# Kernel tuning notes

Hardware: AMD Instinct MI355X
Metric: run time of the kernel (lower is better)

## Reference

```python
import jax, jax.numpy as jnp
import numpy as np

EPS = 1e-5

def splice(x, offsets):
    # x: [B, F, T]; offsets already shifted so offsets[0] == 0.
    # Output channel order matches torch reshape(-1, C*F): y[b, f*C+c, t] = x[b, f, t+off[c]]
    w = offsets[-1]
    Tn = x.shape[2] - w
    y = jnp.stack([x[:, :, o:o + Tn] for o in offsets], axis=2)  # [B, F, C, Tn]
    B, F, C, _ = y.shape
    return y.reshape(B, F * C, Tn)

def conv1x1(x, w, b):
    # x: [B, Cin, T], w: [Cout, Cin], b: [Cout]
    return jnp.einsum('oc,bct->bot', w, x) + b[None, :, None]

def bn_ct(x, gamma=None, beta=None):
    # BatchNorm1d (training mode, biased var) over (batch, time) per channel
    m = x.mean(axis=(0, 2), keepdims=True)
    v = x.var(axis=(0, 2), keepdims=True)
    y = (x - m) * jax.lax.rsqrt(v + EPS)
    if gamma is not None:
        y = y * gamma[None, :, None] + beta[None, :, None]
    return y

def bn_c(x, gamma, beta):
    # BatchNorm1d on [B, C]
    m = x.mean(axis=0, keepdims=True)
    v = x.var(axis=0, keepdims=True)
    return (x - m) * jax.lax.rsqrt(v + EPS) * gamma[None, :] + beta[None, :]

def relu6(x):
    return jnp.clip(x, 0.0, 6.0)

def setup_inputs() -> dict:
    key = jax.random.key(0)
    ks = list(jax.random.split(key, 32))
    def rn(shape, scale=0.05):
        return jax.random.normal(ks.pop(), shape, dtype=jnp.float32) * scale
    inp = {
        'x': jax.random.normal(ks.pop(), (32, 2048, 20), dtype=jnp.float32),
        'h1_w': rn((512, 100)), 'h1_b': rn((512,)),
        'h2_w': rn((512, 1536)), 'h2_b': rn((512,)),
        'bn2_g': jnp.ones((512,), jnp.float32), 'bn2_b': jnp.zeros((512,), jnp.float32),
        'h3_w': rn((512, 1536)), 'h3_b': rn((512,)),
        'bn3_g': jnp.ones((512,), jnp.float32), 'bn3_b': jnp.zeros((512,), jnp.float32),
        'h4_w': rn((512, 512)), 'h4_b': rn((512,)),
        'bn4_g': jnp.ones((512,), jnp.float32), 'bn4_b': jnp.zeros((512,), jnp.float32),
        'h5_w': rn((1500, 512)), 'h5_b': rn((1500,)),
        'bn5_g': jnp.ones((1500,), jnp.float32), 'bn5_b': jnp.zeros((1500,), jnp.float32),
        'l1_w': rn((512, 3000)), 'l1_b': rn((512,)),
        'bn6_g': jnp.ones((512,), jnp.float32), 'bn6_b': jnp.zeros((512,), jnp.float32),
        'l2_w': rn((512, 512)), 'l2_b': rn((512,)),
        'bn7_g': jnp.ones((512,), jnp.float32), 'bn7_b': jnp.zeros((512,), jnp.float32),
    }
    return inp

def reference(x, h1_w, h1_b, h2_w, h2_b, bn2_g, bn2_b, h3_w, h3_b, bn3_g, bn3_b,
              h4_w, h4_b, bn4_g, bn4_b, h5_w, h5_b, bn5_g, bn5_b,
              l1_w, l1_b, bn6_g, bn6_b, l2_w, l2_b, bn7_g, bn7_b):
    o = jnp.transpose(x, (0, 2, 1))                     # [B, 20, T]
    o = splice(o, (0, 1, 2, 3, 4))                      # context [-2..2] -> [B, 100, T-4]
    o = bn_ct(jax.nn.relu(conv1x1(o, h1_w, h1_b)))      # bn1 affine=False
    o = splice(o, (0, 2, 4))                            # context [-2,0,2] -> [B, 1536, T-8]
    o = bn_ct(jax.nn.relu(conv1x1(o, h2_w, h2_b)), bn2_g, bn2_b)
    o = splice(o, (0, 3, 6))                            # context [-3,0,3] -> [B, 1536, T-14]
    o = bn_ct(jax.nn.relu(conv1x1(o, h3_w, h3_b)), bn3_g, bn3_b)
    o = bn_ct(relu6(conv1x1(o, h4_w, h4_b)), bn4_g, bn4_b)
    o = bn_ct(relu6(conv1x1(o, h5_w, h5_b)), bn5_g, bn5_b)  # [B, 1500, T']
    mean = o.mean(axis=-1)
    std = jnp.std(o, axis=-1, ddof=1)                   # torch.std is unbiased
    o = jnp.concatenate((mean, std), axis=1)            # [B, 3000]
    o = bn_c(relu6(o @ l1_w.T + l1_b), bn6_g, bn6_b)
    o = bn_c(relu6(o @ l2_w.T + l2_b), bn7_g, bn7_b)
    return o
```

## Files before the change

### kernel.cpp

```cpp
#include <hip/hip_runtime.h>
#include <cstdint>

#define EPSF 1e-5f

namespace {

typedef _Float16 f16;
typedef _Float16 v8h __attribute__((ext_vector_type(8)));
typedef float v4f __attribute__((ext_vector_type(4)));

constexpr int B  = 32;
constexpr int T0 = 2048, F0 = 20;
constexpr int T1 = 2044, T2 = 2040, T3 = 2034;
constexpr int TS = 2048;

__device__ __forceinline__ void gload16(const void* g, void* l) {
    typedef const __attribute__((address_space(1))) void* gp_t;
    typedef __attribute__((address_space(3))) void* lp_t;
    __builtin_amdgcn_global_load_lds((gp_t)(unsigned long long)g,
                                     (lp_t)(unsigned int)(unsigned long long)l,
                                     16, 0, 0);
}
__device__ __forceinline__ void wait_vm4() { asm volatile("s_waitcnt vmcnt(4)" ::: "memory"); }
__device__ __forceinline__ void wait_vm0() { asm volatile("s_waitcnt vmcnt(0)" ::: "memory"); }

__global__ __launch_bounds__(256) void transpose_x(const float* __restrict__ x,
                                                   f16* __restrict__ xT,
                                                   float* __restrict__ stZ)
{
    int idx = blockIdx.x * 256 + threadIdx.x;
    if (idx < 4096) stZ[idx] = 0.f;
    constexpr int total = B * 3 * TS * 8;
    if (idx >= total) return;
    int fl = idx & 7;
    int t  = (idx >> 3) & (TS - 1);
    int fo = (idx >> 14) % 3;
    int b  = idx / (3 << 14);
    int f  = fo * 8 + fl;
    float v = (f < F0) ? x[((size_t)b * T0 + t) * F0 + f] : 0.f;
    xT[idx] = (f16)v;
}

template<int FP, int C>
__global__ __launch_bounds__(256) void fold_mfma(
    const float* __restrict__ W, const float* __restrict__ bias,
    const float* __restrict__ st, const float* __restrict__ gamma, const float* __restrict__ beta,
    f16* __restrict__ Wh, float* __restrict__ bf,
    int Oreal, int Freal, int Cin, int CinOrig, float invN)
{
    int o = blockIdx.x;
    auto sidx = [&](int k) {
        return ((size_t)((o >> 7) * (Cin >> 3) + (k >> 3)) * 128 + (o & 127)) * 8 + (k & 7);
    };
    if (o >= Oreal) {
        for (int k = threadIdx.x; k < Cin; k += 256) Wh[sidx(k)] = (f16)0.f;
        if (threadIdx.x == 0) bf[o] = 0.f;
        return;
    }
    float local = 0.f;
    for (int k = threadIdx.x; k < Cin; k += 256) {
        int c = k / FP, f = k - c * FP;
        float wv = 0.f;
        if (c < C && f < Freal) {
            float sc = 1.f, sh = 0.f;
            if (st) {
                float mean = st[f] * invN;
                float var  = st[Freal + f] * invN - mean * mean;
                sc = rsqrtf(var + EPSF);
                if (gamma) sc *= gamma[f];
                sh = (beta ? beta[f] : 0.f) - mean * sc;
            }
            float w = W[(size_t)o * CinOrig + f * C + c];
            wv = w * sc;
            local += w * sh;
        }
        Wh[sidx(k)] = (f16)wv;
    }
#pragma unroll
    for (int d = 32; d; d >>= 1) local += __shfl_down(local, d);
    __shared__ float red[4];
    if ((threadIdx.x & 63) == 0) red[threadIdx.x >> 6] = local;
    __syncthreads();
    if (threadIdx.x == 0) bf[o] = bias[o] + red[0] + red[1] + red[2] + red[3];
}

template<int ACT, int FPR, int CIN>
__global__ __launch_bounds__(256, 4) void conv_mfma(
    const f16* __restrict__ inT, const f16* __restrict__ Wh,
    const float* __restrict__ bias, f16* __restrict__ outT,
    float* __restrict__ st, int O, int Tout, int offMul)
{
    __shared__ __align__(16) f16 Ilds[2][4 * 128 * 8];
    __shared__ __align__(16) f16 Wlds[2][4 * 128 * 8];
    __shared__ float redS[2][128];
    __shared__ float redQ[2][128];
    const int tid  = threadIdx.x;
    const int lane = tid & 63, wave = tid >> 6;
    const int wt = wave & 1, wo = wave >> 1;
    const int quad = lane >> 4, l16 = lane & 15;
    const int tB = blockIdx.x * 128, oB = blockIdx.y * 128, b = blockIdx.z;
    const f16* inb = inT + (size_t)b * FPR * TS;
    const size_t wBase = (size_t)(oB >> 7) * (CIN >> 3);

    v4f acc[4][4];
#pragma unroll
    for (int mi = 0; mi < 4; ++mi)
#pragma unroll
        for (int ni = 0; ni < 4; ++ni)
#pragma unroll
            for (int r = 0; r < 4; ++r) acc[mi][ni][r] = 0.f;

    constexpr int nIter = CIN >> 5;

    auto compute = [&](int pb) {
        v8h afr[4], bfr[4];
#pragma unroll
        for (int mi = 0; mi < 4; ++mi)
            afr[mi] = *(const v8h*)&Ilds[pb][(quad * 128 + wt * 64 + mi * 16 + l16) * 8];
#pragma unroll
        for (int ni = 0; ni < 4; ++ni)
            bfr[ni] = *(const v8h*)&Wlds[pb][(quad * 128 + wo * 64 + ni * 16 + l16) * 8];
#pragma unroll
        for (int mi = 0; mi < 4; ++mi)
#pragma unroll
            for (int ni = 0; ni < 4; ++ni)
                acc[mi][ni] = __builtin_amdgcn_mfma_f32_16x16x32_f16(
                    afr[mi], bfr[ni], acc[mi][ni], 0, 0, 0);
    };

    if constexpr (FPR == 512) {
        const char* gp0;
        const char* gp1;
        intptr_t dN, dWr;
        if (wave < 2) {
            gp0 = (const char*)(inb + ((size_t)(2 * wave) * TS + tB + lane) * 8);
            gp1 = gp0 + (size_t)TS * 16;
            dN  = (intptr_t)4 * TS * 16;
            dWr = ((intptr_t)(-60) * TS + offMul) * 16;
        } else {
            gp0 = (const char*)(Wh + ((wBase + 2 * (wave - 2)) * 128 + lane) * 8);
            gp1 = gp0;
            dN  = 8192;
            dWr = 8192;
        }
        auto stage_fast = [&](int pb) {
            f16* Ib = &Ilds[pb][0];
            f16* Wb = &Wlds[pb][0];
            if (wave < 2) {
                int k0 = 2 * wave;
                gload16(gp0,        Ib + (k0 * 128) * 8);
                gload16(gp0 + 1024, Ib + (k0 * 128 + 64) * 8);
                gload16(gp1,        Ib + ((k0 + 1) * 128) * 8);
                gload16(gp1 + 1024, Ib + ((k0 + 1) * 128 + 64) * 8);
            } else {
                int k0 = 2 * (wave - 2);
                gload16(gp0,        Wb + (k0 * 128) * 8);
                gload16(gp0 + 1024, Wb + (k0 * 128 + 64) * 8);
                gload16(gp0 + 2048, Wb + ((k0 + 1) * 128) * 8);
                gload16(gp0 + 3072, Wb + ((k0 + 1) * 128 + 64) * 8);
            }
        };
        auto advance = [&](int kFrom) {
            intptr_t d = (((kFrom + 1) & 15) == 0) ? dWr : dN;
            gp0 += d;
            if (wave < 2) gp1 += d;
        };

        stage_fast(0);
        advance(0);
#pragma unroll 2
        for (int k = 0; k < nIter; ++k) {
            const int pb = k & 1;
            __syncthreads();
            if (k + 1 < nIter) { stage_fast(pb ^ 1); advance(k + 1); wait_vm4(); }
            else               { wait_vm0(); }
            __syncthreads();
            compute(pb);
        }
    } else {
        auto stage = [&](int iB, int pb) {
#pragma unroll
            for (int j = 0; j < 4; ++j) {
                int s = wave * 4 + j;
                int koct = (s & 7) >> 1, half = s & 1;
                if (s < 8) {
                    int kidx = iB + koct * 8;
                    int c = kidx / FPR, f = kidx - c * FPR;
                    int t = tB + half * 64 + lane + c * offMul;
                    gload16(inb + ((size_t)(f >> 3) * TS + t) * 8,
                            &Ilds[pb][(koct * 128 + half * 64) * 8]);
                } else {
                    gload16(Wh + ((wBase + (iB >> 3) + koct) * 128 + half * 64 + lane) * 8,
                            &Wlds[pb][(koct * 128 + half * 64) * 8]);
                }
            }
        };
        stage(0, 0);
#pragma unroll 2
        for (int k = 0; k < nIter; ++k) {
            const int pb = k & 1;
            __syncthreads();
            if (k + 1 < nIter) { stage((k + 1) * 32, pb ^ 1); wait_vm4(); }
            else               { wait_vm0(); }
            __syncthreads();
            compute(pb);
        }
    }

    float Sl[4] = {0, 0, 0, 0}, Ql[4] = {0, 0, 0, 0};
#pragma unroll
    for (int ni = 0; ni < 4; ++ni) {
        const int o  = oB + wo * 64 + ni * 16 + l16;
        const float bs = bias[o];
        f16* orow = outT + (size_t)b * O * TS + (size_t)(o >> 3) * TS * 8 + (o & 7);
#pragma unroll
        for (int mi = 0; mi < 4; ++mi)
#pragma unroll
            for (int r = 0; r < 4; ++r) {
                int t = tB + wt * 64 + mi * 16 + quad * 4 + r;
                if (t < Tout) {
                    float v = acc[mi][ni][r] + bs;
                    v = fmaxf(v, 0.f);
                    if (ACT == 2) v = fminf(v, 6.f);
                    orow[(size_t)t * 8] = (f16)v;
                    Sl[ni] += v; Ql[ni] += v * v;
                }
            }
    }
#pragma unroll
    for (int ni = 0; ni < 4; ++ni) {
        float s = Sl[ni], q = Ql[ni];
        s += __shfl_down(s, 32); q += __shfl_down(q, 32);
        s += __shfl_down(s, 16); q += __shfl_down(q, 16);
        if (lane < 16) {
            redS[wt][wo * 64 + ni * 16 + lane] = s;
            redQ[wt][wo * 64 + ni * 16 + lane] = q;
        }
    }
    __syncthreads();
    if (tid < 128) {
        atomicAdd(&st[oB + tid],       redS[0][tid] + redS[1][tid]);
        atomicAdd(&st[512 + oB + tid], redQ[0][tid] + redQ[1][tid]);
    }
}

template<int CIN>
__global__ __launch_bounds__(256, 4) void pool_mfma(
    const f16* __restrict__ inT, const f16* __restrict__ Wh,
    const float* __restrict__ bias, float* __restrict__ Sp, float* __restrict__ Qp,
    int T, int Opad)
{
    const int L    = blockIdx.x;
    const int slot = L >> 3;
    const int oB   = (slot % 12) * 128;
    const int cz   = (L & 7) + 8 * (slot / 12);
    const int b    = cz & 31, z = cz >> 5;

    __shared__ __align__(16) f16 Ilds[2][4 * 128 * 8];
    __shared__ __align__(16) f16 Wlds[2][4 * 128 * 8];
    __shared__ float redS[2][128];
    __shared__ float redQ[2][128];
    const int tid  = threadIdx.x;
    const int lane = tid & 63, wave = tid >> 6;
    const int wt = wave & 1, wo = wave >> 1;
    const int quad = lane >> 4, l16 = lane & 15;
    const f16* inb = inT + (size_t)b * CIN * TS;
    const size_t wBase = (size_t)(oB >> 7) * (CIN >> 3);

    float Sl[4] = {0, 0, 0, 0}, Ql[4] = {0, 0, 0, 0};
    float bs[4];
#pragma unroll
    for (int ni = 0; ni < 4; ++ni) bs[ni] = bias[oB + wo * 64 + ni * 16 + l16];

    const int tBase = z * 256;
    constexpr int kPer  = CIN >> 5;
    constexpr int total = 2 * kPer;

    v4f acc[4][4];
#pragma unroll
    for (int mi = 0; mi < 4; ++mi)
#pragma unroll
        for (int ni = 0; ni < 4; ++ni)
#pragma unroll
            for (int r = 0; r < 4; ++r) acc[mi][ni][r] = 0.f;

    const char* gp0;
    const char* gp1;
    intptr_t dN, dWr;
    if (wave < 2) {
        gp0 = (const char*)(inb + ((size_t)(2 * wave) * TS + tBase + lane) * 8);
        gp1 = gp0 + (size_t)TS * 16;
        dN  = (intptr_t)4 * TS * 16;
        dWr = ((intptr_t)(-60) * TS + 128) * 16;
    } else {
        gp0 = (const char*)(Wh + ((wBase + 2 * (wave - 2)) * 128 + lane) * 8);
        gp1 = gp0;
        dN  = 8192;
        dWr = (intptr_t)(-60) * 128 * 16;
    }
    auto stage_fast = [&](int pb) {
        f16* Ib = &Ilds[pb][0];
        f16* Wb = &Wlds[pb][0];
        if (wave < 2) {
            int k0 = 2 * wave;
            gload16(gp0,        Ib + (k0 * 128) * 8);
            gload16(gp0 + 1024, Ib + (k0 * 128 + 64) * 8);
            gload16(gp1,        Ib + ((k0 + 1) * 128) * 8);
            gload16(gp1 + 1024, Ib + ((k0 + 1) * 128 + 64) * 8);
        } else {
            int k0 = 2 * (wave - 2);
            gload16(gp0,        Wb + (k0 * 128) * 8);
            gload16(gp0 + 1024, Wb + (k0 * 128 + 64) * 8);
            gload16(gp0 + 2048, Wb + ((k0 + 1) * 128) * 8);
            gload16(gp0 + 3072, Wb + ((k0 + 1) * 128 + 64) * 8);
        }
    };
    auto advance = [&](int itFrom) {
        intptr_t d = (((itFrom + 1) & 15) == 0) ? dWr : dN;
        gp0 += d;
        if (wave < 2) gp1 += d;
    };

    stage_fast(0);
    advance(0);
#pragma unroll 2
    for (int it = 0; it < total; ++it) {
        const int pb = it & 1;
        __syncthreads();
        if (it + 1 < total) { stage_fast(pb ^ 1); advance(it + 1); wait_vm4(); }
        else                { wait_vm0(); }
        __syncthreads();
        v8h afr[4], bfr[4];
#pragma unroll
        for (int mi = 0; mi < 4; ++mi)
            afr[mi] = *(const v8h*)&Ilds[pb][(quad * 128 + wt * 64 + mi * 16 + l16) * 8];
#pragma unroll
        for (int ni = 0; ni < 4; ++ni)
            bfr[ni] = *(const v8h*)&Wlds[pb][(quad * 128 + wo * 64 + ni * 16 + l16) * 8];
#pragma unroll
        for (int mi = 0; mi < 4; ++mi)
#pragma unroll
            for (int ni = 0; ni < 4; ++ni)
                acc[mi][ni] = __builtin_amdgcn_mfma_f32_16x16x32_f16(
                    afr[mi], bfr[ni], acc[mi][ni], 0, 0, 0);

        if ((it & (kPer - 1)) == kPer - 1) {
            int tB = tBase + (it >> 4) * 128;
#pragma unroll
            for (int ni = 0; ni < 4; ++ni)
#pragma unroll
                for (int mi = 0; mi < 4; ++mi)
#pragma unroll
                    for (int r = 0; r < 4; ++r) {
                        int t = tB + wt * 64 + mi * 16 + quad * 4 + r;
                        if (t < T) {
                            float v = fminf(fmaxf(acc[mi][ni][r] + bs[ni], 0.f), 6.f);
                            Sl[ni] += v; Ql[ni] += v * v;
                        }
                        acc[mi][ni][r] = 0.f;
                    }
        }
    }

#pragma unroll
    for (int ni = 0; ni < 4; ++ni) {
        float s = Sl[ni], q = Ql[ni];
        s += __shfl_down(s, 32); q += __shfl_down(q, 32);
        s += __shfl_down(s, 16); q += __shfl_down(q, 16);
        if (lane < 16) {
            redS[wt][wo * 64 + ni * 16 + lane] = s;
            redQ[wt][wo * 64 + ni * 16 + lane] = q;
        }
    }
    __syncthreads();
    if (tid < 128) {
        int o = oB + tid;
        Sp[((size_t)z * B + b) * Opad + o] = redS[0][tid] + redS[1][tid];
        Qp[((size_t)z * B + b) * Opad + o] = redQ[0][tid] + redQ[1][tid];
    }
}

__global__ __launch_bounds__(256) void pool_finalize(
    const float* __restrict__ Sp, const float* __restrict__ Qp,
    const float* __restrict__ g5, const float* __restrict__ b5,
    float* __restrict__ stat, int Opad, int Oreal, int T)
{
    int wid  = (blockIdx.x * 256 + threadIdx.x) >> 6;
    int lane = threadIdx.x & 63;
    if (wid >= Oreal) return;
    const int co = wid;
    const int b  = lane & 31, zh = lane >> 5;
    double sb = 0, qb = 0;
#pragma unroll
    for (int zz = 0; zz < 4; ++zz) {
        int z = zh + 2 * zz;
        sb += Sp[((size_t)z * B + b) * Opad + co];
        qb += Qp[((size_t)z * B + b) * Opad + co];
    }
    sb += __shfl_xor(sb, 32);
    qb += __shfl_xor(qb, 32);
    double sS = sb, sQ = qb;
#pragma unroll
    for (int d = 16; d; d >>= 1) { sS += __shfl_xor(sS, d); sQ += __shfl_xor(sQ, d); }
    double invN = 1.0 / ((double)B * T);
    double m = sS * invN;
    double v = sQ * invN - m * m;
    float sc = g5[co] * rsqrtf((float)v + EPSF);
    float sh = b5[co] - (float)m * sc;
    if (lane < 32) {
        double mb = sb / T;
        double vb = (qb - sb * sb / T) / (T - 1);
        if (vb < 0) vb = 0;
        stat[(size_t)b * 2 * Oreal + co]         = (float)mb * sc + sh;
        stat[(size_t)b * 2 * Oreal + Oreal + co] = sqrtf((float)vb) * fabsf(sc);
    }
}

__global__ __launch_bounds__(256) void fc_relu6(const float* __restrict__ x,
                                                const float* __restrict__ W,
                                                const float* __restrict__ bias,
                                                float* __restrict__ y, int Cin, int O)
{
    int wid = (blockIdx.x * 256 + threadIdx.x) >> 6;
    int lane = threadIdx.x & 63;
    if (wid >= B * O) return;
    int b = wid / O, o = wid - b * O;
    const float* xr = x + (size_t)b * Cin;
    const float* wr = W + (size_t)o * Cin;
    float s = 0.f;
    for (int c = lane; c < Cin; c += 64) s = fmaf(xr[c], wr[c], s);
#pragma unroll
    for (int d = 32; d; d >>= 1) s += __shfl_down(s, d);
    if (lane == 0) y[wid] = fminf(fmaxf(s + bias[o], 0.f), 6.f);
}

__global__ __launch_bounds__(512) void bn_batch(const float* __restrict__ x,
                                                const float* __restrict__ g,
                                                const float* __restrict__ be,
                                                float* __restrict__ y, int O)
{
    int o = threadIdx.x;
    if (o >= O) return;
    float s = 0.f, q = 0.f;
    for (int b = 0; b < B; ++b) { float v = x[b * O + o]; s += v; q += v * v; }
    float m = s / B;
    float var = q / B - m * m;
    float sc = g[o] * rsqrtf(var + EPSF);
    float sh = be[o] - m * sc;
    for (int b = 0; b < B; ++b) y[b * O + o] = x[b * O + o] * sc + sh;
}

}

extern "C" void kernel_launch(void* const* d_in, const int* in_sizes, int n_in,
                              void* d_out, int out_size, void* d_ws, size_t ws_size,
                              hipStream_t stream)
{
    (void)in_sizes; (void)n_in; (void)out_size; (void)ws_size;
    const float* x     = (const float*)d_in[0];
    const float* h1_w  = (const float*)d_in[1];
    const float* h1_b  = (const float*)d_in[2];
    const float* h2_w  = (const float*)d_in[3];
    const float* h2_b  = (const float*)d_in[4];
    const float* bn2_g = (const float*)d_in[5];
    const float* bn2_b = (const float*)d_in[6];
    const float* h3_w  = (const float*)d_in[7];
    const float* h3_b  = (const float*)d_in[8];
    const float* bn3_g = (const float*)d_in[9];
    const float* bn3_b = (const float*)d_in[10];
    const float* h4_w  = (const float*)d_in[11];
    const float* h4_b  = (const float*)d_in[12];
    const float* bn4_g = (const float*)d_in[13];
    const float* bn4_b = (const float*)d_in[14];
    const float* h5_w  = (const float*)d_in[15];
    const float* h5_b  = (const float*)d_in[16];
    const float* bn5_g = (const float*)d_in[17];
    const float* bn5_b = (const float*)d_in[18];
    const float* l1_w  = (const float*)d_in[19];
    const float* l1_b  = (const float*)d_in[20];
    const float* bn6_g = (const float*)d_in[21];
    const float* bn6_b = (const float*)d_in[22];
    const float* l2_w  = (const float*)d_in[23];
    const float* l2_b  = (const float*)d_in[24];
    const float* bn7_g = (const float*)d_in[25];
    const float* bn7_b = (const float*)d_in[26];

    char* ws = (char*)d_ws;
    size_t off = 0;
    auto alloc = [&](size_t bytes) {
        char* p = ws + off;
        off += (bytes + 255) & ~(size_t)255;
        return (void*)p;
    };
    f16* xT    = (f16*)alloc(((size_t)B * 3  * TS * 8 + 2048) * 2);
    f16* bufA  = (f16*)alloc(((size_t)B * 64 * TS * 8 + 2048) * 2);
    f16* bufB  = (f16*)alloc(((size_t)B * 64 * TS * 8 + 2048) * 2);
    f16* Wh1   = (f16*)alloc((size_t)512 * 128 * 2);
    f16* Wh2   = (f16*)alloc((size_t)512 * 1536 * 2);
    f16* Wh3   = (f16*)alloc((size_t)512 * 1536 * 2);
    f16* Wh4   = (f16*)alloc((size_t)512 * 512 * 2);
    f16* Wh5   = (f16*)alloc((size_t)1536 * 512 * 2);
    float* bf1 = (float*)alloc(512 * 4);
    float* bf2 = (float*)alloc(512 * 4);
    float* bf3 = (float*)alloc(512 * 4);
    float* bf4 = (float*)alloc(512 * 4);
    float* bf5 = (float*)alloc(1536 * 4);
    float* stZ = (float*)alloc(4096 * 4);
    float* st1 = stZ, *st2 = stZ + 1024, *st3 = stZ + 2048, *st4 = stZ + 3072;
    float* Sp  = (float*)alloc((size_t)8 * B * 1536 * 4);
    float* Qp  = (float*)alloc((size_t)8 * B * 1536 * 4);
    float* stat = (float*)alloc((size_t)B * 3000 * 4);
    float* f1  = (float*)alloc((size_t)B * 512 * 4);
    float* f2  = (float*)alloc((size_t)B * 512 * 4);

    transpose_x<<<(B * 3 * TS * 8 + 255) / 256, 256, 0, stream>>>(x, xT, stZ);

    fold_mfma<24, 5><<<512, 256, 0, stream>>>(h1_w, h1_b, nullptr, nullptr, nullptr,
                                              Wh1, bf1, 512, 20, 128, 100, 0.f);
    conv_mfma<1, 24, 128><<<dim3(16, 4, B), 256, 0, stream>>>(
        xT, Wh1, bf1, bufA, st1, 512, T1, 1);

    fold_mfma<512, 3><<<512, 256, 0, stream>>>(h2_w, h2_b, st1, nullptr, nullptr,
                                               Wh2, bf2, 512, 512, 1536, 1536,
                                               1.f / (B * T1));
    conv_mfma<1, 512, 1536><<<dim3(16, 4, B), 256, 0, stream>>>(
        bufA, Wh2, bf2, bufB, st2, 512, T2, 2);

    fold_mfma<512, 3><<<512, 256, 0, stream>>>(h3_w, h3_b, st2, bn2_g, bn2_b,
                                               Wh3, bf3, 512, 512, 1536, 1536,
                                               1.f / (B * T2));
    conv_mfma<1, 512, 1536><<<dim3(16, 4, B), 256, 0, stream>>>(
        bufB, Wh3, bf3, bufA, st3, 512, T3, 3);

    fold_mfma<512, 1><<<512, 256, 0, stream>>>(h4_w, h4_b, st3, bn3_g, bn3_b,
                                               Wh4, bf4, 512, 512, 512, 512,
                                               1.f / (B * T3));
    conv_mfma<2, 512, 512><<<dim3(16, 4, B), 256, 0, stream>>>(
        bufA, Wh4, bf4, bufB, st4, 512, T3, 0);

    fold_mfma<512, 1><<<1536, 256, 0, stream>>>(h5_w, h5_b, st4, bn4_g, bn4_b,
                                                Wh5, bf5, 1500, 512, 512, 512,
                                                1.f / (B * T3));
    pool_mfma<512><<<3072, 256, 0, stream>>>(bufB, Wh5, bf5, Sp, Qp, T3, 1536);

    pool_finalize<<<(1500 * 64 + 255) / 256, 256, 0, stream>>>(
        Sp, Qp, bn5_g, bn5_b, stat, 1536, 1500, T3);

    fc_relu6<<<(B * 512 * 64 + 255) / 256, 256, 0, stream>>>(stat, l1_w, l1_b, f1, 3000, 512);
    bn_batch<<<1, 512, 0, stream>>>(f1, bn6_g, bn6_b, f1, 512);
    fc_relu6<<<(B * 512 * 64 + 255) / 256, 256, 0, stream>>>(f1, l2_w, l2_b, f2, 512, 512);
    bn_batch<<<1, 512, 0, stream>>>(f2, bn7_g, bn7_b, (float*)d_out, 512);
}
```

Baseline: 641.6 us.

## Load MFMA operands directly from global memory into registers, bypassing LDS staging

Adds conv_reg and pool_reg kernels where each wave loads its A and W fragments straight from global memory into registers. This replaces the double-buffered global_load_lds staging with its two barriers per iteration. The 512-channel layers and the pooling layer now use these kernels. The conv_mfma fast path is removed, and conv_mfma stays only for layer 1. This removes the LDS traffic and barrier stalls, but each wave now loads its own copy of data the block previously shared, so global and L2 traffic rise and latency hiding depends on unrolling.

```diff
diff --git a/kernel.cpp b/kernel.cpp
--- a/kernel.cpp
+++ b/kernel.cpp
@@ -128,83 +128,32 @@
                     afr[mi], bfr[ni], acc[mi][ni], 0, 0, 0);
     };
 
-    if constexpr (FPR == 512) {
-        const char* gp0;
-        const char* gp1;
-        intptr_t dN, dWr;
-        if (wave < 2) {
-            gp0 = (const char*)(inb + ((size_t)(2 * wave) * TS + tB + lane) * 8);
-            gp1 = gp0 + (size_t)TS * 16;
-            dN  = (intptr_t)4 * TS * 16;
-            dWr = ((intptr_t)(-60) * TS + offMul) * 16;
-        } else {
-            gp0 = (const char*)(Wh + ((wBase + 2 * (wave - 2)) * 128 + lane) * 8);
-            gp1 = gp0;
-            dN  = 8192;
-            dWr = 8192;
+    auto stage = [&](int iB, int pb) {
+#pragma unroll
+        for (int j = 0; j < 4; ++j) {
+            int s = wave * 4 + j;
+            int koct = (s & 7) >> 1, half = s & 1;
+            if (s < 8) {
+                int kidx = iB + koct * 8;
+                int c = kidx / FPR, f = kidx - c * FPR;
+                int t = tB + half * 64 + lane + c * offMul;
+                gload16(inb + ((size_t)(f >> 3) * TS + t) * 8,
+                        &Ilds[pb][(koct * 128 + half * 64) * 8]);
+            } else {
+                gload16(Wh + ((wBase + (iB >> 3) + koct) * 128 + half * 64 + lane) * 8,
+                        &Wlds[pb][(koct * 128 + half * 64) * 8]);
+            }
         }
-        auto stage_fast = [&](int pb) {
-            f16* Ib = &Ilds[pb][0];
-            f16* Wb = &Wlds[pb][0];
-            if (wave < 2) {
-                int k0 = 2 * wave;
-                gload16(gp0,        Ib + (k0 * 128) * 8);
-                gload16(gp0 + 1024, Ib + (k0 * 128 + 64) * 8);
-                gload16(gp1,        Ib + ((k0 + 1) * 128) * 8);
-                gload16(gp1 + 1024, Ib + ((k0 + 1) * 128 + 64) * 8);
-            } else {
-                int k0 = 2 * (wave - 2);
-                gload16(gp0,        Wb + (k0 * 128) * 8);
-                gload16(gp0 + 1024, Wb + (k0 * 128 + 64) * 8);
-                gload16(gp0 + 2048, Wb + ((k0 + 1) * 128) * 8);
-                gload16(gp0 + 3072, Wb + ((k0 + 1) * 128 + 64) * 8);
-            }
-        };
-        auto advance = [&](int kFrom) {
-            intptr_t d = (((kFrom + 1) & 15) == 0) ? dWr : dN;
-            gp0 += d;
-            if (wave < 2) gp1 += d;
-        };
-
-        stage_fast(0);
-        advance(0);
+    };
+    stage(0, 0);
 #pragma unroll 2
-        for (int k = 0; k < nIter; ++k) {
-            const int pb = k & 1;
-            __syncthreads();
-            if (k + 1 < nIter) { stage_fast(pb ^ 1); advance(k + 1); wait_vm4(); }
-            else               { wait_vm0(); }
-            __syncthreads();
-            compute(pb);
-        }
-    } else {
-        auto stage = [&](int iB, int pb) {
-#pragma unroll
-            for (int j = 0; j < 4; ++j) {
-                int s = wave * 4 + j;
-                int koct = (s & 7) >> 1, half = s & 1;
-                if (s < 8) {
-                    int kidx = iB + koct * 8;
-                    int c = kidx / FPR, f = kidx - c * FPR;
-                    int t = tB + half * 64 + lane + c * offMul;
-                    gload16(inb + ((size_t)(f >> 3) * TS + t) * 8,
-                            &Ilds[pb][(koct * 128 + half * 64) * 8]);
-                } else {
-                    gload16(Wh + ((wBase + (iB >> 3) + koct) * 128 + half * 64 + lane) * 8,
-                            &Wlds[pb][(koct * 128 + half * 64) * 8]);
-                }
-            }
-        };
-        stage(0, 0);
-#pragma unroll 2
-        for (int k = 0; k < nIter; ++k) {
-            const int pb = k & 1;
-            __syncthreads();
-            if (k + 1 < nIter) { stage((k + 1) * 32, pb ^ 1); wait_vm4(); }
-            else               { wait_vm0(); }
-            __syncthreads();
-            compute(pb);
-        }
+    for (int k = 0; k < nIter; ++k) {
+        const int pb = k & 1;
+        __syncthreads();
+        if (k + 1 < nIter) { stage((k + 1) * 32, pb ^ 1); wait_vm4(); }
+        else               { wait_vm0(); }
+        __syncthreads();
+        compute(pb);
     }
 
     float Sl[4] = {0, 0, 0, 0}, Ql[4] = {0, 0, 0, 0};
@@ -244,8 +193,96 @@
     }
 }
 
+template<int ACT, int CIN>
+__global__ __launch_bounds__(256, 4) void conv_reg(
+    const f16* __restrict__ inT, const f16* __restrict__ Wh,
+    const float* __restrict__ bias, f16* __restrict__ outT,
+    float* __restrict__ st, int O, int Tout, int offMul)
+{
+    __shared__ float redS[2][128];
+    __shared__ float redQ[2][128];
+    const int tid  = threadIdx.x;
+    const int lane = tid & 63, wave = tid >> 6;
+    const int wt = wave & 1, wo = wave >> 1;
+    const int quad = lane >> 4, l16 = lane & 15;
+    const int tB = blockIdx.x * 128, oB = blockIdx.y * 128, b = blockIdx.z;
+    const f16* inb = inT + (size_t)b * 64 * TS * 8;
+    const size_t wBase = (size_t)(oB >> 7) * (CIN >> 3);
+
+    v4f acc[4][4];
+#pragma unroll
+    for (int mi = 0; mi < 4; ++mi)
+#pragma unroll
+        for (int ni = 0; ni < 4; ++ni)
+#pragma unroll
+            for (int r = 0; r < 4; ++r) acc[mi][ni][r] = 0.f;
+
+    constexpr int nIter = CIN >> 5;
+
+    const f16* pA = inb + ((size_t)quad * TS + tB + wt * 64 + l16) * 8;
+    const f16* pW = Wh + ((wBase + quad) * 128 + wo * 64 + l16) * 8;
+    const intptr_t dA  = (intptr_t)4 * TS * 8;
+    const intptr_t dAw = ((intptr_t)(-60) * TS + offMul) * 8;
+    const intptr_t dW  = (intptr_t)4 * 128 * 8;
+
+#pragma unroll 4
+    for (int k = 0; k < nIter; ++k) {
+        v8h a[4], w[4];
+#pragma unroll
+        for (int mi = 0; mi < 4; ++mi)
+            a[mi] = *(const v8h*)(pA + mi * 128);
+#pragma unroll
+        for (int ni = 0; ni < 4; ++ni)
+            w[ni] = *(const v8h*)(pW + ni * 128);
+#pragma unroll
+        for (int mi = 0; mi < 4; ++mi)
+#pragma unroll
+            for (int ni = 0; ni < 4; ++ni)
+                acc[mi][ni] = __builtin_amdgcn_mfma_f32_16x16x32_f16(
+                    a[mi], w[ni], acc[mi][ni], 0, 0, 0);
+        pA += (CIN == 1536 && ((k + 1) & 15) == 0) ? dAw : dA;
+        pW += dW;
+    }
+
+    float Sl[4] = {0, 0, 0, 0}, Ql[4] = {0, 0, 0, 0};
+#pragma unroll
+    for (int ni = 0; ni < 4; ++ni) {
+        const int o  = oB + wo * 64 + ni * 16 + l16;
+        const float bs = bias[o];
+        f16* orow = outT + (size_t)b * O * TS + (size_t)(o >> 3) * TS * 8 + (o & 7);
+#pragma unroll
+        for (int mi = 0; mi < 4; ++mi)
+#pragma unroll
+            for (int r = 0; r < 4; ++r) {
+                int t = tB + wt * 64 + mi * 16 + quad * 4 + r;
+                if (t < Tout) {
+                    float v = acc[mi][ni][r] + bs;
+                    v = fmaxf(v, 0.f);
+                    if (ACT == 2) v = fminf(v, 6.f);
+                    orow[(size_t)t * 8] = (f16)v;
+                    Sl[ni] += v; Ql[ni] += v * v;
+                }
+            }
+    }
+#pragma unroll
+    for (int ni = 0; ni < 4; ++ni) {
+        float s = Sl[ni], q = Ql[ni];
+        s += __shfl_down(s, 32); q += __shfl_down(q, 32);
+        s += __shfl_down(s, 16); q += __shfl_down(q, 16);
+        if (lane < 16) {
+            redS[wt][wo * 64 + ni * 16 + lane] = s;
+            redQ[wt][wo * 64 + ni * 16 + lane] = q;
+        }
+    }
+    __syncthreads();
+    if (tid < 128) {
+        atomicAdd(&st[oB + tid],       redS[0][tid] + redS[1][tid]);
+        atomicAdd(&st[512 + oB + tid], redQ[0][tid] + redQ[1][tid]);
+    }
+}
+
 template<int CIN>
-__global__ __launch_bounds__(256, 4) void pool_mfma(
+__global__ __launch_bounds__(256, 4) void pool_reg(
     const f16* __restrict__ inT, const f16* __restrict__ Wh,
     const float* __restrict__ bias, float* __restrict__ Sp, float* __restrict__ Qp,
     int T, int Opad)
@@ -256,8 +293,6 @@
     const int cz   = (L & 7) + 8 * (slot / 12);
     const int b    = cz & 31, z = cz >> 5;
 
-    __shared__ __align__(16) f16 Ilds[2][4 * 128 * 8];
-    __shared__ __align__(16) f16 Wlds[2][4 * 128 * 8];
     __shared__ float redS[2][128];
     __shared__ float redQ[2][128];
     const int tid  = threadIdx.x;
@@ -273,93 +308,54 @@
     for (int ni = 0; ni < 4; ++ni) bs[ni] = bias[oB + wo * 64 + ni * 16 + l16];
 
     const int tBase = z * 256;
-    constexpr int kPer  = CIN >> 5;
-    constexpr int total = 2 * kPer;
-
-    v4f acc[4][4];
-#pragma unroll
-    for (int mi = 0; mi < 4; ++mi)
+    constexpr int kPer = CIN >> 5;
+    const intptr_t dA = (intptr_t)4 * TS * 8;
+    const intptr_t dW = (intptr_t)4 * 128 * 8;
+
+    for (int ch = 0; ch < 2; ++ch) {
+        const int tC = tBase + ch * 128;
+        const f16* pA = inb + ((size_t)quad * TS + tC + wt * 64 + l16) * 8;
+        const f16* pW = Wh + ((wBase + quad) * 128 + wo * 64 + l16) * 8;
+
+        v4f acc[4][4];
+#pragma unroll
+        for (int mi = 0; mi < 4; ++mi)
+#pragma unroll
+            for (int ni = 0; ni < 4; ++ni)
+#pragma unroll
+                for (int r = 0; r < 4; ++r) acc[mi][ni][r] = 0.f;
+
+#pragma unroll 4
+        for (int k = 0; k < kPer; ++k) {
+            v8h a[4], w[4];
+#pragma unroll
+            for (int mi = 0; mi < 4; ++mi)
+                a[mi] = *(const v8h*)(pA + mi * 128);
+#pragma unroll
+            for (int ni = 0; ni < 4; ++ni)
+                w[ni] = *(const v8h*)(pW + ni * 128);
+#pragma unroll
+            for (int mi = 0; mi < 4; ++mi)
+#pragma unroll
+                for (int ni = 0; ni < 4; ++ni)
+                    acc[mi][ni] = __builtin_amdgcn_mfma_f32_16x16x32_f16(
+                        a[mi], w[ni], acc[mi][ni], 0, 0, 0);
+            pA += dA;
+            pW += dW;
+        }
+
 #pragma unroll
         for (int ni = 0; ni < 4; ++ni)
 #pragma unroll
-            for (int r = 0; r < 4; ++r) acc[mi][ni][r] = 0.f;
-
-    const char* gp0;
-    const char* gp1;
-    intptr_t dN, dWr;
-    if (wave < 2) {
-        gp0 = (const char*)(inb + ((size_t)(2 * wave) * TS + tBase + lane) * 8);
-        gp1 = gp0 + (size_t)TS * 16;
-        dN  = (intptr_t)4 * TS * 16;
-        dWr = ((intptr_t)(-60) * TS + 128) * 16;
-    } else {
-        gp0 = (const char*)(Wh + ((wBase + 2 * (wave - 2)) * 128 + lane) * 8);
-        gp1 = gp0;
-        dN  = 8192;
-        dWr = (intptr_t)(-60) * 128 * 16;
-    }
-    auto stage_fast = [&](int pb) {
-        f16* Ib = &Ilds[pb][0];
-        f16* Wb = &Wlds[pb][0];
-        if (wave < 2) {
-            int k0 = 2 * wave;
-            gload16(gp0,        Ib + (k0 * 128) * 8);
-            gload16(gp0 + 1024, Ib + (k0 * 128 + 64) * 8);
-            gload16(gp1,        Ib + ((k0 + 1) * 128) * 8);
-            gload16(gp1 + 1024, Ib + ((k0 + 1) * 128 + 64) * 8);
-        } else {
-            int k0 = 2 * (wave - 2);
-            gload16(gp0,        Wb + (k0 * 128) * 8);
-            gload16(gp0 + 1024, Wb + (k0 * 128 + 64) * 8);
-            gload16(gp0 + 2048, Wb + ((k0 + 1) * 128) * 8);
-            gload16(gp0 + 3072, Wb + ((k0 + 1) * 128 + 64) * 8);
-        }
-    };
-    auto advance = [&](int itFrom) {
-        intptr_t d = (((itFrom + 1) & 15) == 0) ? dWr : dN;
-        gp0 += d;
-        if (wave < 2) gp1 += d;
-    };
-
-    stage_fast(0);
-    advance(0);
-#pragma unroll 2
-    for (int it = 0; it < total; ++it) {
-        const int pb = it & 1;
-        __syncthreads();
-        if (it + 1 < total) { stage_fast(pb ^ 1); advance(it + 1); wait_vm4(); }
-        else                { wait_vm0(); }
-        __syncthreads();
-        v8h afr[4], bfr[4];
-#pragma unroll
-        for (int mi = 0; mi < 4; ++mi)
-            afr[mi] = *(const v8h*)&Ilds[pb][(quad * 128 + wt * 64 + mi * 16 + l16) * 8];
-#pragma unroll
-        for (int ni = 0; ni < 4; ++ni)
-            bfr[ni] = *(const v8h*)&Wlds[pb][(quad * 128 + wo * 64 + ni * 16 + l16) * 8];
-#pragma unroll
-        for (int mi = 0; mi < 4; ++mi)
-#pragma unroll
-            for (int ni = 0; ni < 4; ++ni)
-                acc[mi][ni] = __builtin_amdgcn_mfma_f32_16x16x32_f16(
-                    afr[mi], bfr[ni], acc[mi][ni], 0, 0, 0);
-
-        if ((it & (kPer - 1)) == kPer - 1) {
-            int tB = tBase + (it >> 4) * 128;
-#pragma unroll
-            for (int ni = 0; ni < 4; ++ni)
-#pragma unroll
-                for (int mi = 0; mi < 4; ++mi)
-#pragma unroll
-                    for (int r = 0; r < 4; ++r) {
-                        int t = tB + wt * 64 + mi * 16 + quad * 4 + r;
-                        if (t < T) {
-                            float v = fminf(fmaxf(acc[mi][ni][r] + bs[ni], 0.f), 6.f);
-                            Sl[ni] += v; Ql[ni] += v * v;
-                        }
-                        acc[mi][ni][r] = 0.f;
+            for (int mi = 0; mi < 4; ++mi)
+#pragma unroll
+                for (int r = 0; r < 4; ++r) {
+                    int t = tC + wt * 64 + mi * 16 + quad * 4 + r;
+                    if (t < T) {
+                        float v = fminf(fmaxf(acc[mi][ni][r] + bs[ni], 0.f), 6.f);
+                        Sl[ni] += v; Ql[ni] += v * v;
                     }
-        }
+                }
     }
 
 #pragma unroll
@@ -523,25 +519,25 @@
     fold_mfma<512, 3><<<512, 256, 0, stream>>>(h2_w, h2_b, st1, nullptr, nullptr,
                                                Wh2, bf2, 512, 512, 1536, 1536,
                                                1.f / (B * T1));
-    conv_mfma<1, 512, 1536><<<dim3(16, 4, B), 256, 0, stream>>>(
+    conv_reg<1, 1536><<<dim3(16, 4, B), 256, 0, stream>>>(
         bufA, Wh2, bf2, bufB, st2, 512, T2, 2);
 
     fold_mfma<512, 3><<<512, 256, 0, stream>>>(h3_w, h3_b, st2, bn2_g, bn2_b,
                                                Wh3, bf3, 512, 512, 1536, 1536,
                                                1.f / (B * T2));
-    conv_mfma<1, 512, 1536><<<dim3(16, 4, B), 256, 0, stream>>>(
+    conv_reg<1, 1536><<<dim3(16, 4, B), 256, 0, stream>>>(
         bufB, Wh3, bf3, bufA, st3, 512, T3, 3);
 
     fold_mfma<512, 1><<<512, 256, 0, stream>>>(h4_w, h4_b, st3, bn3_g, bn3_b,
                                                Wh4, bf4, 512, 512, 512, 512,
                                                1.f / (B * T3));
-    conv_mfma<2, 512, 512><<<dim3(16, 4, B), 256, 0, stream>>>(
+    conv_reg<2, 512><<<dim3(16, 4, B), 256, 0, stream>>>(
         bufA, Wh4, bf4, bufB, st4, 512, T3, 0);
 
     fold_mfma<512, 1><<<1536, 256, 0, stream>>>(h5_w, h5_b, st4, bn4_g, bn4_b,
                                                 Wh5, bf5, 1500, 512, 512, 512,
                                                 1.f / (B * T3));
-    pool_mfma<512><<<3072, 256, 0, stream>>>(bufB, Wh5, bf5, Sp, Qp, T3, 1536);
+    pool_reg<512><<<3072, 256, 0, stream>>>(bufB, Wh5, bf5, Sp, Qp, T3, 1536);
 
     pool_finalize<<<(1500 * 64 + 255) / 256, 256, 0, stream>>>(
         Sp, Qp, bn5_g, bn5_b, stat, 1536, 1500, T3);
```

New measurement: 670.1 us. +4.4%, slower.
